# Performance work log

Measured on AMD Instinct MI355X. Metric: run time of the kernel, lower is better.

Reference implementation:

```python
import jax, jax.numpy as jnp
import numpy as np

N = 50000      # nodes
E = 800000     # edges (avg degree 16)
F0 = 3         # node feature dim
EF = 3         # edge feature dim
C = 4          # num classes


def _lin_params(k, din, dout):
    k1, k2 = jax.random.split(k)
    s = 1.0 / np.sqrt(din)
    W = jax.random.uniform(k1, (dout, din), jnp.float32, -s, s)
    b = jax.random.uniform(k2, (dout,), jnp.float32, -s, s)
    return W, b


def setup_inputs() -> dict:
    key = jax.random.key(0)
    ks = jax.random.split(key, 8)
    x = jax.random.normal(ks[0], (N, F0), jnp.float32)
    edge_index = jax.random.randint(ks[1], (2, E), 0, N, jnp.int32)
    edge_attr = jax.random.uniform(ks[2], (E, EF), dtype=jnp.float32)
    W1, b1 = _lin_params(ks[3], 2 * F0 + EF, 128)
    W2, b2 = _lin_params(ks[4], 2 * 128 + EF, 64)
    W3, b3 = _lin_params(ks[5], 2 * 64 + EF, 32)
    Wc, bc = _lin_params(ks[6], 32, C)
    return dict(x=x, edge_index=edge_index, edge_attr=edge_attr,
                W1=W1, b1=b1, W2=W2, b2=b2, W3=W3, b3=b3, Wc=Wc, bc=bc)


def _edgeconv(x, src, dst, ea, W, b, n):
    # message = Linear(cat([x_i, x_j, edge_attr])); aggregated by scatter-add to dst (x_i side).
    # Split W so the node-side matmuls happen once per node instead of per edge.
    f = x.shape[1]
    Wi, Wj, We = W[:, :f], W[:, f:2 * f], W[:, 2 * f:]
    ai = x @ Wi.T   # [N, out]
    aj = x @ Wj.T   # [N, out]
    msg = ai[dst] + aj[src] + ea @ We.T + b  # [E_aug, out]
    return jax.ops.segment_sum(msg, dst, num_segments=n)


def reference(x, edge_index, edge_attr, W1, b1, W2, b2, W3, b3, Wc, bc):
    n = x.shape[0]
    loops = jnp.arange(n, dtype=edge_index.dtype)
    src = jnp.concatenate([edge_index[0], loops])  # x_j indices
    dst = jnp.concatenate([edge_index[1], loops])  # x_i indices (aggregation targets)
    ea = jnp.concatenate([edge_attr, jnp.zeros((n, edge_attr.shape[1]), edge_attr.dtype)])
    h = jax.nn.relu(_edgeconv(x, src, dst, ea, W1, b1, n))
    h = jax.nn.relu(_edgeconv(h, src, dst, ea, W2, b2, n))
    h = _edgeconv(h, src, dst, ea, W3, b3, n)  # no relu after conv3 in the original
    logits = h @ Wc.T + bc
    return jax.nn.log_softmax(logits, axis=1)
```

## Files before the change

### kernel.cpp

```cpp
#include <hip/hip_runtime.h>
#include <math.h>


static inline size_t align256(size_t x) { return (x + 255) & ~size_t(255); }

typedef unsigned short ushort_t;
using frag8  = __attribute__((ext_vector_type(8))) short;
using f32x4v = __attribute__((ext_vector_type(4))) float;
using half8  = __attribute__((ext_vector_type(8))) _Float16;

__device__ inline unsigned short f2bf(float f) {
    unsigned u = __float_as_uint(f);
    unsigned r = (u + 0x7fffu + ((u >> 16) & 1u)) >> 16;
    return (unsigned short)r;
}
__device__ inline float bflo(unsigned u) { return __uint_as_float(u << 16); }
__device__ inline float bfhi(unsigned u) { return __uint_as_float(u & 0xffff0000u); }


__global__ __launch_bounds__(256) void build_count(
    const int* __restrict__ ei, int* __restrict__ count,
    int* __restrict__ pos, int E)
{
    int e4 = (blockIdx.x * 256 + threadIdx.x) * 4;
    if (e4 >= E) return;
    if (e4 + 3 < E) {
        int4 d = *(const int4*)(ei + E + e4);
        int4 po;
        po.x = atomicAdd(&count[d.x], 1);
        po.y = atomicAdd(&count[d.y], 1);
        po.z = atomicAdd(&count[d.z], 1);
        po.w = atomicAdd(&count[d.w], 1);
        *(int4*)(pos + e4) = po;
    } else {
        for (int e = e4; e < E; ++e)
            pos[e] = atomicAdd(&count[ei[E + e]], 1);
    }
}

__global__ __launch_bounds__(256) void scan_pass1(
    const int* __restrict__ count, int* __restrict__ rowstart,
    int* __restrict__ bsum, int n)
{
    __shared__ int sh[256];
    const int tid = threadIdx.x;
    const int base = blockIdx.x * 1024 + tid * 4;
    int v0 = 0, v1 = 0, v2 = 0, v3 = 0;
    if (base + 3 < n) {
        int4 c = *(const int4*)(count + base);
        v0 = c.x; v1 = c.y; v2 = c.z; v3 = c.w;
    } else {
        if (base + 0 < n) v0 = count[base + 0];
        if (base + 1 < n) v1 = count[base + 1];
        if (base + 2 < n) v2 = count[base + 2];
        if (base + 3 < n) v3 = count[base + 3];
    }
    int tsum = v0 + v1 + v2 + v3;
    sh[tid] = tsum;
    __syncthreads();
    for (int off = 1; off < 256; off <<= 1) {
        int t = (tid >= off) ? sh[tid - off] : 0;
        __syncthreads();
        sh[tid] += t;
        __syncthreads();
    }
    int excl = sh[tid] - tsum;
    int p0 = excl + v0, p1 = p0 + v1, p2 = p1 + v2, p3 = p2 + v3;
    if (base + 0 < n) rowstart[base + 1] = p0;
    if (base + 1 < n) rowstart[base + 2] = p1;
    if (base + 2 < n) rowstart[base + 3] = p2;
    if (base + 3 < n) rowstart[base + 4] = p3;
    if (tid == 255) bsum[blockIdx.x] = sh[255];
}

__global__ __launch_bounds__(256) void mid_fused(
    const int* __restrict__ bsum, int* __restrict__ bexcl, int nb,
    const float* __restrict__ W3, const float* __restrict__ b3,
    const float* __restrict__ Wc, const float* __restrict__ bc,
    float* __restrict__ AB, float* __restrict__ consts,
    const float* __restrict__ W2, ushort_t* __restrict__ W2bf)
{
    const int t = threadIdx.x;
    if (blockIdx.x == 0) {
        if (t < 64) {
            int own = (t < nb) ? bsum[t] : 0;
            int x = own;
            for (int off = 1; off < 64; off <<= 1) {
                int s = __shfl_up(x, off);
                if (t >= off) x += s;
            }
            bexcl[t] = x - own;
        }
    } else if (blockIdx.x == 1) {
        for (int idx = t; idx < 512; idx += 256) {
            int j = idx >> 6, k = idx & 63;
            int jj = j & 3;
            int base = (j >= 4) ? 64 : 0;
            float s = 0.f;
            #pragma unroll
            for (int c = 0; c < 32; ++c)
                s += Wc[jj * 32 + c] * W3[c * 131 + base + k];
            AB[idx] = s;
        }
        if (t < 4) {
            float db = 0.f;
            for (int c = 0; c < 32; ++c) db += Wc[t * 32 + c] * b3[c];
            consts[t] = db;
            consts[4 + t] = bc[t];
            for (int q = 0; q < 3; ++q) {
                float s = 0.f;
                for (int c = 0; c < 32; ++c) s += Wc[t * 32 + c] * W3[c * 131 + 128 + q];
                consts[8 + t * 3 + q] = s;
            }
        }
    } else {
        int i0 = (blockIdx.x - 2) * 4096 + t;
        int i1 = (blockIdx.x - 1) * 4096;
        for (int idx = i0; idx < i1; idx += 256) {
            int jg = idx >> 7, k = idx & 127;
            float w = (jg < 64) ? W2[jg * 259 + k] : W2[(jg - 64) * 259 + 128 + k];
            W2bf[idx] = f2bf(w);
        }
    }
}

__global__ __launch_bounds__(256) void scan_pass3(
    int* __restrict__ rowstart, const int* __restrict__ bexcl,
    const float* __restrict__ x, float4* __restrict__ xpad, int n)
{
    int j = blockIdx.x * 256 + threadIdx.x;
    if (j > n) return;
    if (j == 0) {
        rowstart[0] = 0;
    } else {
        int b = (j - 1) >> 10;
        if (b > 0) rowstart[j] += bexcl[b];
    }
    if (j < n)
        xpad[j] = make_float4(x[j * 3], x[j * 3 + 1], x[j * 3 + 2], 0.f);
}

__global__ __launch_bounds__(256) void csr_scatter(
    const int* __restrict__ ei, const float* __restrict__ ea,
    const int* __restrict__ pos, const int* __restrict__ rowstart,
    uint2* __restrict__ csrp, int E)
{
    int e4 = (blockIdx.x * 256 + threadIdx.x) * 4;
    if (e4 >= E) return;
    if (e4 + 3 < E) {
        int4 s = *(const int4*)(ei + e4);
        int4 d = *(const int4*)(ei + E + e4);
        int4 po = *(const int4*)(pos + e4);
        float4 a = *(const float4*)(ea + (size_t)e4 * 3);
        float4 b = *(const float4*)(ea + (size_t)e4 * 3 + 4);
        float4 c = *(const float4*)(ea + (size_t)e4 * 3 + 8);
        float ev[12] = { a.x, a.y, a.z, a.w, b.x, b.y, b.z, b.w, c.x, c.y, c.z, c.w };
        int sv[4] = { s.x, s.y, s.z, s.w };
        int dv[4] = { d.x, d.y, d.z, d.w };
        int pv[4] = { po.x, po.y, po.z, po.w };
        #pragma unroll
        for (int r = 0; r < 4; ++r) {
            uint2 p;
            p.x = (unsigned)f2bf(ev[r * 3 + 0]) | ((unsigned)f2bf(ev[r * 3 + 1]) << 16);
            p.y = (unsigned)f2bf(ev[r * 3 + 2]) | ((unsigned)sv[r] << 16);
            csrp[rowstart[dv[r]] + pv[r]] = p;
        }
    } else {
        for (int e = e4; e < E; ++e) {
            uint2 p;
            p.x = (unsigned)f2bf(ea[e * 3 + 0]) | ((unsigned)f2bf(ea[e * 3 + 1]) << 16);
            p.y = (unsigned)f2bf(ea[e * 3 + 2]) | ((unsigned)ei[e] << 16);
            csrp[rowstart[ei[E + e]] + pos[e]] = p;
        }
    }
}


__global__ __launch_bounds__(256) void h1_gemm(
    const float4* __restrict__ xpad, const float* __restrict__ W1,
    const float* __restrict__ b1, const int* __restrict__ rowstart,
    const uint2* __restrict__ csrp, float4* __restrict__ eagg4,
    const ushort_t* __restrict__ W2bf,
    float* __restrict__ AI2, _Float16* __restrict__ AJ2, int n_nodes)
{
    constexpr int HS = 144;
    __shared__ float sM[10 * 128];
    __shared__ ushort_t sH[64 * HS];

    const int tid = threadIdx.x;
    for (int t = tid; t < 1280; t += 256) {
        int k = t >> 7, c = t & 127;
        sM[t] = (k < 9) ? W1[c * 9 + k] : b1[c];
    }
    __syncthreads();

    const int base = blockIdx.x * 64;
    const int wave = tid >> 6, wl = tid & 63;
    const int grp = wl >> 3, ch8 = wl & 7;

    #pragma unroll
    for (int pass = 0; pass < 2; ++pass) {
        int nl = pass * 32 + wave * 8 + grp;
        int n = base + nl;
        float hv[16];
        if (n < n_nodes) {
            int s0 = rowstart[n], s1 = rowstart[n + 1];
            float xx = 0.f, xy = 0.f, xz = 0.f, ex = 0.f, ey = 0.f, ez = 0.f;
            for (int i = s0 + ch8; i < s1; i += 8) {
                uint2 p = csrp[i];
                int s = (int)(p.y >> 16);
                ex += bflo(p.x); ey += bfhi(p.x); ez += bflo(p.y);
                float4 xv = xpad[s];
                xx += xv.x; xy += xv.y; xz += xv.z;
            }
            #pragma unroll
            for (int off = 1; off < 8; off <<= 1) {
                xx += __shfl_xor(xx, off); xy += __shfl_xor(xy, off); xz += __shfl_xor(xz, off);
                ex += __shfl_xor(ex, off); ey += __shfl_xor(ey, off); ez += __shfl_xor(ez, off);
            }
            float deg = (float)(s1 - s0 + 1);
            float4 xs = xpad[n];
            float v[10] = { deg * xs.x, deg * xs.y, deg * xs.z,
                            xs.x + xx, xs.y + xy, xs.z + xz,
                            ex, ey, ez, deg };
            #pragma unroll
            for (int q = 0; q < 16; ++q) {
                int c = ch8 * 16 + q;
                float h = 0.f;
                #pragma unroll
                for (int k = 0; k < 10; ++k) h += v[k] * sM[k * 128 + c];
                hv[q] = fmaxf(h, 0.f);
            }
            if (ch8 == 0) eagg4[n] = make_float4(ex, ey, ez, 0.f);
        } else {
            #pragma unroll
            for (int q = 0; q < 16; ++q) hv[q] = 0.f;
        }
        #pragma unroll
        for (int g = 0; g < 2; ++g) {
            uint4 u;
            u.x = (unsigned)f2bf(hv[g * 8 + 0]) | ((unsigned)f2bf(hv[g * 8 + 1]) << 16);
            u.y = (unsigned)f2bf(hv[g * 8 + 2]) | ((unsigned)f2bf(hv[g * 8 + 3]) << 16);
            u.z = (unsigned)f2bf(hv[g * 8 + 4]) | ((unsigned)f2bf(hv[g * 8 + 5]) << 16);
            u.w = (unsigned)f2bf(hv[g * 8 + 6]) | ((unsigned)f2bf(hv[g * 8 + 7]) << 16);
            *(uint4*)(sH + nl * HS + ch8 * 16 + g * 8) = u;
        }
    }
    __syncthreads();

    const int m = wl & 15, quad = wl >> 4;

    frag8 a[4];
    #pragma unroll
    for (int ks = 0; ks < 4; ++ks)
        a[ks] = *(const frag8*)(sH + (wave * 16 + m) * HS + ks * 32 + quad * 8);

    f32x4v acc[8];
    #pragma unroll
    for (int t = 0; t < 8; ++t) acc[t] = (f32x4v)(0.f);

    #pragma unroll
    for (int t = 0; t < 8; ++t) {
        #pragma unroll
        for (int ks = 0; ks < 4; ++ks) {
            frag8 b = *(const frag8*)(W2bf + (t * 16 + m) * 128 + ks * 32 + quad * 8);
            acc[t] = __builtin_amdgcn_mfma_f32_16x16x32_bf16(a[ks], b, acc[t], 0, 0, 0);
        }
    }

    #pragma unroll
    for (int reg = 0; reg < 4; ++reg) {
        int grow = base + wave * 16 + quad * 4 + reg;
        if (grow >= n_nodes) continue;
        #pragma unroll
        for (int t = 0; t < 4; ++t)
            AI2[(size_t)grow * 64 + t * 16 + m] = acc[t][reg];
        #pragma unroll
        for (int t = 4; t < 8; ++t)
            AJ2[(size_t)grow * 64 + (t - 4) * 16 + m] = (_Float16)acc[t][reg];
    }
}


__global__ __launch_bounds__(256) void gather2(
    const float* __restrict__ AI2, const _Float16* __restrict__ AJ2,
    const float* __restrict__ W2, const float* __restrict__ b2,
    const float4* __restrict__ eagg4, const int* __restrict__ rowstart,
    const uint2* __restrict__ csrp, const float* __restrict__ AB,
    float* __restrict__ U, float* __restrict__ Z, int n_nodes)
{
    __shared__ float sAB[512];
    __shared__ float sWe[192];
    const int tid = threadIdx.x;
    for (int t = tid; t < 512; t += 256) sAB[t] = AB[t];
    for (int t = tid; t < 192; t += 256) {
        int c = t / 3, q = t % 3;
        sWe[t] = W2[c * 259 + 256 + q];
    }
    __syncthreads();

    int wl = tid & 63;
    int grp = wl >> 3, ch8 = wl & 7;
    int n = blockIdx.x * 32 + (tid >> 6) * 8 + grp;
    if (n >= n_nodes) return;

    int s0 = rowstart[n], s1 = rowstart[n + 1];

    half8 hacc0 = (half8)(_Float16)0.f;
    half8 hacc1 = (half8)(_Float16)0.f;
    for (int base = s0; base < s1; base += 8) {
        int j = base + ch8;
        if (j >= s1) j = s1 - 1;
        int myidx = (int)(csrp[j].y >> 16);
        int cnt = s1 - base; if (cnt > 8) cnt = 8;
        #pragma unroll
        for (int k = 0; k < 8; ++k) {
            int s = __shfl(myidx, grp * 8 + k);
            if (k < cnt) {
                half8 v = *(const half8*)(AJ2 + (size_t)s * 64 + ch8 * 8);
                if (k & 1) hacc1 += v; else hacc0 += v;
            }
        }
    }
    float acc[8];
    #pragma unroll
    for (int q = 0; q < 8; ++q) acc[q] = (float)hacc0[q] + (float)hacc1[q];

    float deg = (float)(s1 - s0 + 1);
    float4 e4 = eagg4[n];
    const float* aip = AI2 + (size_t)n * 64 + ch8 * 8;
    float4 aiA = *(const float4*)(aip);
    float4 aiB = *(const float4*)(aip + 4);
    half8 su = *(const half8*)(AJ2 + (size_t)n * 64 + ch8 * 8);
    float4 bA = *(const float4*)(b2 + ch8 * 8);
    float4 bB = *(const float4*)(b2 + ch8 * 8 + 4);
    float av[8] = { aiA.x, aiA.y, aiA.z, aiA.w, aiB.x, aiB.y, aiB.z, aiB.w };
    float bv[8] = { bA.x, bA.y, bA.z, bA.w, bB.x, bB.y, bB.z, bB.w };
    float r[8];
    #pragma unroll
    for (int q = 0; q < 8; ++q) {
        int c = ch8 * 8 + q;
        float we = sWe[c * 3] * e4.x + sWe[c * 3 + 1] * e4.y + sWe[c * 3 + 2] * e4.z;
        r[q] = fmaxf(deg * (av[q] + bv[q]) + (float)su[q] + we + acc[q], 0.f);
    }
    float pj[8];
    #pragma unroll
    for (int j = 0; j < 8; ++j) {
        float4 wA = *(const float4*)(sAB + j * 64 + ch8 * 8);
        float4 wB = *(const float4*)(sAB + j * 64 + ch8 * 8 + 4);
        pj[j] = r[0] * wA.x + r[1] * wA.y + r[2] * wA.z + r[3] * wA.w
              + r[4] * wB.x + r[5] * wB.y + r[6] * wB.z + r[7] * wB.w;
    }
    #pragma unroll
    for (int off = 1; off < 8; off <<= 1)
        #pragma unroll
        for (int j = 0; j < 8; ++j) pj[j] += __shfl_xor(pj[j], off);

    if (ch8 == 0) {
        *(float4*)(U + (size_t)n * 4) = make_float4(pj[0], pj[1], pj[2], pj[3]);
        *(float4*)(Z + (size_t)n * 4) = make_float4(pj[4], pj[5], pj[6], pj[7]);
    }
}


__global__ __launch_bounds__(256) void final_softmax(
    const float* __restrict__ U, const float* __restrict__ Z,
    const float4* __restrict__ eagg4, const int* __restrict__ rowstart,
    const uint2* __restrict__ csrp, const float* __restrict__ consts,
    float* __restrict__ out, int n_nodes)
{
    int wl = threadIdx.x & 63;
    int grp = wl >> 3, ch8 = wl & 7;
    int n = blockIdx.x * 32 + (threadIdx.x >> 6) * 8 + grp;
    if (n >= n_nodes) return;

    int s0 = rowstart[n], s1 = rowstart[n + 1];
    float ax = 0.f, ay = 0.f, az = 0.f, aw = 0.f;
    for (int i = s0 + ch8; i < s1; i += 8) {
        int s = (int)(csrp[i].y >> 16);
        float4 z = *(const float4*)(Z + (size_t)s * 4);
        ax += z.x; ay += z.y; az += z.z; aw += z.w;
    }
    #pragma unroll
    for (int off = 1; off < 8; off <<= 1) {
        ax += __shfl_xor(ax, off); ay += __shfl_xor(ay, off);
        az += __shfl_xor(az, off); aw += __shfl_xor(aw, off);
    }
    if (ch8 != 0) return;

    float deg = (float)(s1 - s0 + 1);
    float4 u = *(const float4*)(U + (size_t)n * 4);
    float4 zs = *(const float4*)(Z + (size_t)n * 4);
    float4 e4 = eagg4[n];
    float av[4] = { ax + zs.x, ay + zs.y, az + zs.z, aw + zs.w };
    float uv[4] = { u.x, u.y, u.z, u.w };
    float lg[4];
    #pragma unroll
    for (int j = 0; j < 4; ++j) {
        lg[j] = deg * (uv[j] + consts[j]) + av[j] + consts[4 + j]
              + consts[8 + j * 3] * e4.x + consts[9 + j * 3] * e4.y
              + consts[10 + j * 3] * e4.z;
    }
    float m = fmaxf(fmaxf(lg[0], lg[1]), fmaxf(lg[2], lg[3]));
    float lse = logf(expf(lg[0] - m) + expf(lg[1] - m) + expf(lg[2] - m) + expf(lg[3] - m));
    *(float4*)(out + (size_t)n * 4) =
        make_float4(lg[0] - m - lse, lg[1] - m - lse, lg[2] - m - lse, lg[3] - m - lse);
}


extern "C" void kernel_launch(void* const* d_in, const int* in_sizes, int n_in,
                              void* d_out, int out_size, void* d_ws, size_t ws_size,
                              hipStream_t stream)
{
    const float* x    = (const float*)d_in[0];
    const int*   ei   = (const int*)  d_in[1];
    const float* ea   = (const float*)d_in[2];
    const float* W1   = (const float*)d_in[3];
    const float* b1   = (const float*)d_in[4];
    const float* W2   = (const float*)d_in[5];
    const float* b2   = (const float*)d_in[6];
    const float* W3   = (const float*)d_in[7];
    const float* b3   = (const float*)d_in[8];
    const float* Wc   = (const float*)d_in[9];
    const float* bc   = (const float*)d_in[10];
    float* out = (float*)d_out;

    const int N = in_sizes[0] / 3;
    const int E = in_sizes[1] / 2;

    char* ws = (char*)d_ws;
    size_t off = 0;
    int*    count    = (int*)(ws + off);            off = align256(off + (size_t)N * 4);
    int*    pos      = (int*)(ws + off);            off = align256(off + (size_t)E * 4);
    int*    rowstart = (int*)(ws + off);            off = align256(off + (size_t)(N + 1) * 4);
    uint2*  csrp     = (uint2*)(ws + off);          off = align256(off + (size_t)E * 8);
    int*    bsum     = (int*)(ws + off);            off = align256(off + 256);
    int*    bexcl    = (int*)(ws + off);            off = align256(off + 256);
    float*  AB       = (float*)(ws + off);          off = align256(off + 512 * 4);
    float*  consts   = (float*)(ws + off);          off = align256(off + 32 * 4);
    ushort_t* W2bf   = (ushort_t*)(ws + off);       off = align256(off + 128 * 128 * 2);
    float4* xpad     = (float4*)(ws + off);         off = align256(off + (size_t)N * 16);
    float4* eagg4    = (float4*)(ws + off);         off = align256(off + (size_t)N * 16);
    float*  AI2      = (float*)(ws + off);          off = align256(off + (size_t)N * 64 * 4);
    _Float16* AJ2    = (_Float16*)(ws + off);       off = align256(off + (size_t)N * 64 * 2);
    float*  Ubuf     = (float*)(ws + off);          off = align256(off + (size_t)N * 16);
    float*  Zbuf     = (float*)(ws + off);          off = align256(off + (size_t)N * 16);
    (void)ws_size;

    hipMemsetAsync(count, 0, (size_t)N * 4, stream);

    const int eb4 = ((E + 3) / 4 + 255) / 256;
    build_count<<<eb4, 256, 0, stream>>>(ei, count, pos, E);

    const int nb1 = (N + 1023) / 1024;
    scan_pass1<<<nb1, 256, 0, stream>>>(count, rowstart, bsum, N);
    mid_fused<<<6, 256, 0, stream>>>(bsum, bexcl, nb1, W3, b3, Wc, bc, AB, consts, W2, W2bf);
    scan_pass3<<<(N + 1 + 255) / 256, 256, 0, stream>>>(rowstart, bexcl, x, xpad, N);
    csr_scatter<<<eb4, 256, 0, stream>>>(ei, ea, pos, rowstart, csrp, E);

    h1_gemm<<<(N + 63) / 64, 256, 0, stream>>>(xpad, W1, b1, rowstart, csrp,
                                               eagg4, W2bf, AI2, AJ2, N);

    const int gb = (N + 31) / 32;
    gather2<<<gb, 256, 0, stream>>>(AI2, AJ2, W2, b2, eagg4, rowstart, csrp, AB, Ubuf, Zbuf, N);

    final_softmax<<<gb, 256, 0, stream>>>(Ubuf, Zbuf, eagg4, rowstart, csrp, consts, out, N);
}
```

Before: 205.0 us.

## Merge preprocessing launches and fold block-offset scan into CSR scatter

Fuses the edge count, x padding, W2 bf16 conversion and classifier constant precompute into one prep kernel. The second-level block scan and rowstart finalisation move into the CSR scatter kernel, which rebuilds the block prefix in shared memory and writes a separate finalised rowstart array. This removes the mid_fused and scan_pass3 launches. The b2 bias is also folded into AI2 at h1_gemm output, so gather2 no longer loads it. The aim is to cut launch count and serialization, at the cost of an extra rowstart buffer and a redundant small scan per block.

```diff
diff --git a/kernel.cpp b/kernel.cpp
--- a/kernel.cpp
+++ b/kernel.cpp
@@ -18,25 +18,73 @@
 __device__ inline float bfhi(unsigned u) { return __uint_as_float(u & 0xffff0000u); }
 
 
-__global__ __launch_bounds__(256) void build_count(
+__global__ __launch_bounds__(256) void prep(
     const int* __restrict__ ei, int* __restrict__ count,
-    int* __restrict__ pos, int E)
-{
-    int e4 = (blockIdx.x * 256 + threadIdx.x) * 4;
-    if (e4 >= E) return;
-    if (e4 + 3 < E) {
-        int4 d = *(const int4*)(ei + E + e4);
-        int4 po;
-        po.x = atomicAdd(&count[d.x], 1);
-        po.y = atomicAdd(&count[d.y], 1);
-        po.z = atomicAdd(&count[d.z], 1);
-        po.w = atomicAdd(&count[d.w], 1);
-        *(int4*)(pos + e4) = po;
+    int* __restrict__ pos, int E,
+    const float* __restrict__ x, float4* __restrict__ xpad, int n,
+    const float* __restrict__ W2, ushort_t* __restrict__ W2bf,
+    const float* __restrict__ W3, const float* __restrict__ b3,
+    const float* __restrict__ Wc, const float* __restrict__ bc,
+    float* __restrict__ AB, float* __restrict__ consts,
+    int eb4, int nxb)
+{
+    const int t = threadIdx.x;
+    const int b = blockIdx.x;
+    if (b < eb4) {
+        int e4 = (b * 256 + t) * 4;
+        if (e4 >= E) return;
+        if (e4 + 3 < E) {
+            int4 d = *(const int4*)(ei + E + e4);
+            int4 po;
+            po.x = atomicAdd(&count[d.x], 1);
+            po.y = atomicAdd(&count[d.y], 1);
+            po.z = atomicAdd(&count[d.z], 1);
+            po.w = atomicAdd(&count[d.w], 1);
+            *(int4*)(pos + e4) = po;
+        } else {
+            for (int e = e4; e < E; ++e)
+                pos[e] = atomicAdd(&count[ei[E + e]], 1);
+        }
+    } else if (b < eb4 + nxb) {
+        int j = (b - eb4) * 256 + t;
+        if (j < n) {
+            const float* xp = x + (size_t)j * 3;
+            xpad[j] = make_float4(xp[0], xp[1], xp[2], 0.f);
+        }
+    } else if (b < eb4 + nxb + 4) {
+        int wb = b - (eb4 + nxb);
+        int i0 = wb * 4096 + t;
+        int i1 = (wb + 1) * 4096;
+        for (int idx = i0; idx < i1; idx += 256) {
+            int jg = idx >> 7, k = idx & 127;
+            float w = (jg < 64) ? W2[jg * 259 + k] : W2[(jg - 64) * 259 + 128 + k];
+            W2bf[idx] = f2bf(w);
+        }
     } else {
-        for (int e = e4; e < E; ++e)
-            pos[e] = atomicAdd(&count[ei[E + e]], 1);
-    }
-}
+        for (int idx = t; idx < 512; idx += 256) {
+            int j = idx >> 6, k = idx & 63;
+            int jj = j & 3;
+            int base = (j >= 4) ? 64 : 0;
+            float s = 0.f;
+            #pragma unroll
+            for (int c = 0; c < 32; ++c)
+                s += Wc[jj * 32 + c] * W3[c * 131 + base + k];
+            AB[idx] = s;
+        }
+        if (t < 4) {
+            float db = 0.f;
+            for (int c = 0; c < 32; ++c) db += Wc[t * 32 + c] * b3[c];
+            consts[t] = db;
+            consts[4 + t] = bc[t];
+            for (int q = 0; q < 3; ++q) {
+                float s = 0.f;
+                for (int c = 0; c < 32; ++c) s += Wc[t * 32 + c] * W3[c * 131 + 128 + q];
+                consts[8 + t * 3 + q] = s;
+            }
+        }
+    }
+}
+
 
 __global__ __launch_bounds__(256) void scan_pass1(
     const int* __restrict__ count, int* __restrict__ rowstart,
@@ -73,112 +121,73 @@
     if (tid == 255) bsum[blockIdx.x] = sh[255];
 }
 
-__global__ __launch_bounds__(256) void mid_fused(
-    const int* __restrict__ bsum, int* __restrict__ bexcl, int nb,
-    const float* __restrict__ W3, const float* __restrict__ b3,
-    const float* __restrict__ Wc, const float* __restrict__ bc,
-    float* __restrict__ AB, float* __restrict__ consts,
-    const float* __restrict__ W2, ushort_t* __restrict__ W2bf)
-{
-    const int t = threadIdx.x;
-    if (blockIdx.x == 0) {
-        if (t < 64) {
-            int own = (t < nb) ? bsum[t] : 0;
-            int x = own;
-            for (int off = 1; off < 64; off <<= 1) {
-                int s = __shfl_up(x, off);
-                if (t >= off) x += s;
-            }
-            bexcl[t] = x - own;
-        }
-    } else if (blockIdx.x == 1) {
-        for (int idx = t; idx < 512; idx += 256) {
-            int j = idx >> 6, k = idx & 63;
-            int jj = j & 3;
-            int base = (j >= 4) ? 64 : 0;
-            float s = 0.f;
-            #pragma unroll
-            for (int c = 0; c < 32; ++c)
-                s += Wc[jj * 32 + c] * W3[c * 131 + base + k];
-            AB[idx] = s;
-        }
-        if (t < 4) {
-            float db = 0.f;
-            for (int c = 0; c < 32; ++c) db += Wc[t * 32 + c] * b3[c];
-            consts[t] = db;
-            consts[4 + t] = bc[t];
-            for (int q = 0; q < 3; ++q) {
-                float s = 0.f;
-                for (int c = 0; c < 32; ++c) s += Wc[t * 32 + c] * W3[c * 131 + 128 + q];
-                consts[8 + t * 3 + q] = s;
-            }
-        }
-    } else {
-        int i0 = (blockIdx.x - 2) * 4096 + t;
-        int i1 = (blockIdx.x - 1) * 4096;
-        for (int idx = i0; idx < i1; idx += 256) {
-            int jg = idx >> 7, k = idx & 127;
-            float w = (jg < 64) ? W2[jg * 259 + k] : W2[(jg - 64) * 259 + 128 + k];
-            W2bf[idx] = f2bf(w);
-        }
-    }
-}
-
-__global__ __launch_bounds__(256) void scan_pass3(
-    int* __restrict__ rowstart, const int* __restrict__ bexcl,
-    const float* __restrict__ x, float4* __restrict__ xpad, int n)
-{
-    int j = blockIdx.x * 256 + threadIdx.x;
-    if (j > n) return;
-    if (j == 0) {
-        rowstart[0] = 0;
-    } else {
-        int b = (j - 1) >> 10;
-        if (b > 0) rowstart[j] += bexcl[b];
-    }
-    if (j < n)
-        xpad[j] = make_float4(x[j * 3], x[j * 3 + 1], x[j * 3 + 2], 0.f);
-}
-
-__global__ __launch_bounds__(256) void csr_scatter(
+
+__global__ __launch_bounds__(256) void csr_scatter2(
     const int* __restrict__ ei, const float* __restrict__ ea,
     const int* __restrict__ pos, const int* __restrict__ rowstart,
-    uint2* __restrict__ csrp, int E)
-{
-    int e4 = (blockIdx.x * 256 + threadIdx.x) * 4;
-    if (e4 >= E) return;
-    if (e4 + 3 < E) {
-        int4 s = *(const int4*)(ei + e4);
-        int4 d = *(const int4*)(ei + E + e4);
-        int4 po = *(const int4*)(pos + e4);
-        float4 a = *(const float4*)(ea + (size_t)e4 * 3);
-        float4 b = *(const float4*)(ea + (size_t)e4 * 3 + 4);
-        float4 c = *(const float4*)(ea + (size_t)e4 * 3 + 8);
-        float ev[12] = { a.x, a.y, a.z, a.w, b.x, b.y, b.z, b.w, c.x, c.y, c.z, c.w };
-        int sv[4] = { s.x, s.y, s.z, s.w };
-        int dv[4] = { d.x, d.y, d.z, d.w };
-        int pv[4] = { po.x, po.y, po.z, po.w };
-        #pragma unroll
-        for (int r = 0; r < 4; ++r) {
-            uint2 p;
-            p.x = (unsigned)f2bf(ev[r * 3 + 0]) | ((unsigned)f2bf(ev[r * 3 + 1]) << 16);
-            p.y = (unsigned)f2bf(ev[r * 3 + 2]) | ((unsigned)sv[r] << 16);
-            csrp[rowstart[dv[r]] + pv[r]] = p;
+    const int* __restrict__ bsum, int nb,
+    uint2* __restrict__ csrp, int* __restrict__ rowfin,
+    int E, int n, int eb4)
+{
+    __shared__ int sBex[64];
+    const int tid = threadIdx.x;
+    if (tid < 64) {
+        int v = (tid < nb) ? bsum[tid] : 0;
+        int xx = v;
+        #pragma unroll
+        for (int off = 1; off < 64; off <<= 1) {
+            int t = __shfl_up(xx, off);
+            if (tid >= off) xx += t;
+        }
+        sBex[tid] = xx - v;
+    }
+    __syncthreads();
+
+    if (blockIdx.x < eb4) {
+        int e4 = (blockIdx.x * 256 + tid) * 4;
+        if (e4 >= E) return;
+        if (e4 + 3 < E) {
+            int4 s = *(const int4*)(ei + e4);
+            int4 d = *(const int4*)(ei + E + e4);
+            int4 po = *(const int4*)(pos + e4);
+            float4 a = *(const float4*)(ea + (size_t)e4 * 3);
+            float4 bq = *(const float4*)(ea + (size_t)e4 * 3 + 4);
+            float4 c = *(const float4*)(ea + (size_t)e4 * 3 + 8);
+            float ev[12] = { a.x, a.y, a.z, a.w, bq.x, bq.y, bq.z, bq.w, c.x, c.y, c.z, c.w };
+            int sv[4] = { s.x, s.y, s.z, s.w };
+            int dv[4] = { d.x, d.y, d.z, d.w };
+            int pv[4] = { po.x, po.y, po.z, po.w };
+            #pragma unroll
+            for (int r = 0; r < 4; ++r) {
+                uint2 p;
+                p.x = (unsigned)f2bf(ev[r * 3 + 0]) | ((unsigned)f2bf(ev[r * 3 + 1]) << 16);
+                p.y = (unsigned)f2bf(ev[r * 3 + 2]) | ((unsigned)sv[r] << 16);
+                int dd = dv[r];
+                int rs = (dd == 0) ? 0 : (rowstart[dd] + sBex[(dd - 1) >> 10]);
+                csrp[rs + pv[r]] = p;
+            }
+        } else {
+            for (int e = e4; e < E; ++e) {
+                uint2 p;
+                p.x = (unsigned)f2bf(ea[e * 3 + 0]) | ((unsigned)f2bf(ea[e * 3 + 1]) << 16);
+                p.y = (unsigned)f2bf(ea[e * 3 + 2]) | ((unsigned)ei[e] << 16);
+                int dd = ei[E + e];
+                int rs = (dd == 0) ? 0 : (rowstart[dd] + sBex[(dd - 1) >> 10]);
+                csrp[rs + pos[e]] = p;
+            }
         }
     } else {
-        for (int e = e4; e < E; ++e) {
-            uint2 p;
-            p.x = (unsigned)f2bf(ea[e * 3 + 0]) | ((unsigned)f2bf(ea[e * 3 + 1]) << 16);
-            p.y = (unsigned)f2bf(ea[e * 3 + 2]) | ((unsigned)ei[e] << 16);
-            csrp[rowstart[ei[E + e]] + pos[e]] = p;
-        }
+        int j = (blockIdx.x - eb4) * 256 + tid;
+        if (j <= n)
+            rowfin[j] = (j == 0) ? 0 : (rowstart[j] + sBex[(j - 1) >> 10]);
     }
 }
 
 
 __global__ __launch_bounds__(256) void h1_gemm(
     const float4* __restrict__ xpad, const float* __restrict__ W1,
-    const float* __restrict__ b1, const int* __restrict__ rowstart,
+    const float* __restrict__ b1, const float* __restrict__ b2,
+    const int* __restrict__ rowstart,
     const uint2* __restrict__ csrp, float4* __restrict__ eagg4,
     const ushort_t* __restrict__ W2bf,
     float* __restrict__ AI2, _Float16* __restrict__ AJ2, int n_nodes)
@@ -268,13 +277,17 @@
         }
     }
 
+    float b2v[4];
+    #pragma unroll
+    for (int t = 0; t < 4; ++t) b2v[t] = b2[t * 16 + m];
+
     #pragma unroll
     for (int reg = 0; reg < 4; ++reg) {
         int grow = base + wave * 16 + quad * 4 + reg;
         if (grow >= n_nodes) continue;
         #pragma unroll
         for (int t = 0; t < 4; ++t)
-            AI2[(size_t)grow * 64 + t * 16 + m] = acc[t][reg];
+            AI2[(size_t)grow * 64 + t * 16 + m] = acc[t][reg] + b2v[t];
         #pragma unroll
         for (int t = 4; t < 8; ++t)
             AJ2[(size_t)grow * 64 + (t - 4) * 16 + m] = (_Float16)acc[t][reg];
@@ -284,7 +297,7 @@
 
 __global__ __launch_bounds__(256) void gather2(
     const float* __restrict__ AI2, const _Float16* __restrict__ AJ2,
-    const float* __restrict__ W2, const float* __restrict__ b2,
+    const float* __restrict__ W2,
     const float4* __restrict__ eagg4, const int* __restrict__ rowstart,
     const uint2* __restrict__ csrp, const float* __restrict__ AB,
     float* __restrict__ U, float* __restrict__ Z, int n_nodes)
@@ -332,16 +345,13 @@
     float4 aiA = *(const float4*)(aip);
     float4 aiB = *(const float4*)(aip + 4);
     half8 su = *(const half8*)(AJ2 + (size_t)n * 64 + ch8 * 8);
-    float4 bA = *(const float4*)(b2 + ch8 * 8);
-    float4 bB = *(const float4*)(b2 + ch8 * 8 + 4);
     float av[8] = { aiA.x, aiA.y, aiA.z, aiA.w, aiB.x, aiB.y, aiB.z, aiB.w };
-    float bv[8] = { bA.x, bA.y, bA.z, bA.w, bB.x, bB.y, bB.z, bB.w };
     float r[8];
     #pragma unroll
     for (int q = 0; q < 8; ++q) {
         int c = ch8 * 8 + q;
         float we = sWe[c * 3] * e4.x + sWe[c * 3 + 1] * e4.y + sWe[c * 3 + 2] * e4.z;
-        r[q] = fmaxf(deg * (av[q] + bv[q]) + (float)su[q] + we + acc[q], 0.f);
+        r[q] = fmaxf(deg * av[q] + (float)su[q] + we + acc[q], 0.f);
     }
     float pj[8];
     #pragma unroll
@@ -433,9 +443,9 @@
     int*    count    = (int*)(ws + off);            off = align256(off + (size_t)N * 4);
     int*    pos      = (int*)(ws + off);            off = align256(off + (size_t)E * 4);
     int*    rowstart = (int*)(ws + off);            off = align256(off + (size_t)(N + 1) * 4);
+    int*    rowfin   = (int*)(ws + off);            off = align256(off + (size_t)(N + 1) * 4);
     uint2*  csrp     = (uint2*)(ws + off);          off = align256(off + (size_t)E * 8);
     int*    bsum     = (int*)(ws + off);            off = align256(off + 256);
-    int*    bexcl    = (int*)(ws + off);            off = align256(off + 256);
     float*  AB       = (float*)(ws + off);          off = align256(off + 512 * 4);
     float*  consts   = (float*)(ws + off);          off = align256(off + 32 * 4);
     ushort_t* W2bf   = (ushort_t*)(ws + off);       off = align256(off + 128 * 128 * 2);
@@ -450,19 +460,25 @@
     hipMemsetAsync(count, 0, (size_t)N * 4, stream);
 
     const int eb4 = ((E + 3) / 4 + 255) / 256;
-    build_count<<<eb4, 256, 0, stream>>>(ei, count, pos, E);
-
+    const int nxb = (N + 255) / 256;
     const int nb1 = (N + 1023) / 1024;
+    const int nfb = (N + 1 + 255) / 256;
+
+    prep<<<eb4 + nxb + 5, 256, 0, stream>>>(ei, count, pos, E,
+                                            x, xpad, N, W2, W2bf,
+                                            W3, b3, Wc, bc, AB, consts,
+                                            eb4, nxb);
+
     scan_pass1<<<nb1, 256, 0, stream>>>(count, rowstart, bsum, N);
-    mid_fused<<<6, 256, 0, stream>>>(bsum, bexcl, nb1, W3, b3, Wc, bc, AB, consts, W2, W2bf);
-    scan_pass3<<<(N + 1 + 255) / 256, 256, 0, stream>>>(rowstart, bexcl, x, xpad, N);
-    csr_scatter<<<eb4, 256, 0, stream>>>(ei, ea, pos, rowstart, csrp, E);
-
-    h1_gemm<<<(N + 63) / 64, 256, 0, stream>>>(xpad, W1, b1, rowstart, csrp,
+
+    csr_scatter2<<<eb4 + nfb, 256, 0, stream>>>(ei, ea, pos, rowstart, bsum, nb1,
+                                                csrp, rowfin, E, N, eb4);
+
+    h1_gemm<<<(N + 63) / 64, 256, 0, stream>>>(xpad, W1, b1, b2, rowfin, csrp,
                                                eagg4, W2bf, AI2, AJ2, N);
 
     const int gb = (N + 31) / 32;
-    gather2<<<gb, 256, 0, stream>>>(AI2, AJ2, W2, b2, eagg4, rowstart, csrp, AB, Ubuf, Zbuf, N);
-
-    final_softmax<<<gb, 256, 0, stream>>>(Ubuf, Zbuf, eagg4, rowstart, csrp, consts, out, N);
-}
+    gather2<<<gb, 256, 0, stream>>>(AI2, AJ2, W2, eagg4, rowfin, csrp, AB, Ubuf, Zbuf, N);
+
+    final_softmax<<<gb, 256, 0, stream>>>(Ubuf, Zbuf, eagg4, rowfin, csrp, consts, out, N);
+}
```

Result: faster. 198.1 us (-3.4%).
